# Kernel optimization log

Hardware: AMD Instinct MI355X
Metric: run time of the kernel (lower is better)

The kernel has to match this reference:

```python
import jax, jax.numpy as jnp
import numpy as np

N = 50000          # points
K = 16             # neighbors per query (n_max)
M = N * K          # ragged pair count
DIM = 96
HEADS = 6
HEAD_DIM = DIM // HEADS
WINDOW = 4.0
QUANT = 0.25
QGL = int(WINDOW / QUANT)   # quant_grid_length = 16
SCALE = HEAD_DIM ** -0.5


def setup_inputs() -> dict:
    key = jax.random.key(0)
    ks = jax.random.split(key, 10)
    feats = jax.random.normal(ks[0], (N, DIM), dtype=jnp.float32)
    xyz = jax.random.uniform(ks[1], (N, 3), dtype=jnp.float32) * 8.0
    index_0 = jnp.repeat(jnp.arange(N, dtype=jnp.int32), K)            # sorted query ids
    index_1 = jax.random.randint(ks[2], (M,), 0, N, dtype=jnp.int32)   # neighbor ids
    index_0_offsets = jnp.arange(N + 1, dtype=jnp.int32) * K
    W_qkv = jax.random.normal(ks[3], (DIM, 3 * DIM), dtype=jnp.float32) * 0.02
    b_qkv = jnp.zeros((3 * DIM,), dtype=jnp.float32)
    table_q = jax.random.normal(ks[4], (4 * QGL, HEADS, HEAD_DIM, 3), dtype=jnp.float32) * 0.02
    table_k = jax.random.normal(ks[5], (4 * QGL, HEADS, HEAD_DIM, 3), dtype=jnp.float32) * 0.02
    table_v = jax.random.normal(ks[6], (4 * QGL, HEADS, HEAD_DIM, 3), dtype=jnp.float32) * 0.02
    W_proj = jax.random.normal(ks[7], (DIM, DIM), dtype=jnp.float32) * 0.02
    b_proj = jnp.zeros((DIM,), dtype=jnp.float32)
    return {
        "feats": feats, "xyz": xyz,
        "index_0": index_0, "index_0_offsets": index_0_offsets, "n_max": K,
        "index_1": index_1, "shift_size": jnp.float32(0.0),
        "W_qkv": W_qkv, "b_qkv": b_qkv,
        "table_q": table_q, "table_k": table_k, "table_v": table_v,
        "W_proj": W_proj, "b_proj": b_proj,
    }


def reference(feats, xyz, index_0, index_0_offsets, n_max, index_1, shift_size,
              W_qkv, b_qkv, table_q, table_k, table_v, W_proj, b_proj):
    n = feats.shape[0]
    # qkv projection -> (N, 3, H, HD)
    qkv = (feats @ W_qkv + b_qkv).reshape(n, 3, HEADS, HEAD_DIM)
    q = qkv[:, 0] * SCALE
    k = qkv[:, 1]
    v = qkv[:, 2]

    # step1: per-pair QK dot product (pointops.attention_step1_v2)
    qg = q[index_0]                      # (M, H, HD) gathered by query id
    kg = k[index_1]                      # (M, H, HD) gathered by neighbor id
    attn = jnp.einsum('mhd,mhd->mh', qg, kg)   # (M, H)

    # quantized relative positions
    xyz_quant = jnp.floor(((xyz - xyz.min(axis=0) + shift_size) % WINDOW) / QUANT)
    rel = xyz_quant[index_0] - xyz_quant[index_1]       # (M, 3)
    rel_idx = (rel + (QGL - 1)).astype(jnp.int32)       # map_func, in [0, 2*QGL-2]

    # relative position bias (pointops.dot_prod_with_idx_v3: query + key tables)
    bias = jnp.zeros_like(attn)
    for c in range(3):   # fixed 3 coordinate axes
        tq = table_q[rel_idx[:, c], :, :, c]            # (M, H, HD)
        tk = table_k[rel_idx[:, c], :, :, c]
        bias = bias + jnp.einsum('mhd,mhd->mh', qg, tq) + jnp.einsum('mhd,mhd->mh', kg, tk)
    attn = attn + bias

    # scatter softmax over index_0 segments
    seg_max = jax.ops.segment_max(attn, index_0, num_segments=n)
    e = jnp.exp(attn - seg_max[index_0])
    denom = jax.ops.segment_sum(e, index_0, num_segments=n)
    sm = e / denom[index_0]                              # (M, H)

    # step2 with relative position value (pointops.attention_step2_with_rel_pos_value_v2)
    vg = v[index_1]                                      # (M, H, HD)
    for c in range(3):
        vg = vg + table_v[rel_idx[:, c], :, :, c]
    x = jax.ops.segment_sum(sm[:, :, None] * vg, index_0, num_segments=n)  # (N, H, HD)
    x = x.reshape(n, DIM)
    return x @ W_proj + b_proj
```

## Files before the change

### kernel.cpp

```cpp
#include <hip/hip_runtime.h>
#include <hip/hip_fp16.h>
#include <math.h>

#define FLT_BIG 3.402823466e38f
typedef unsigned int uint;
typedef unsigned short ushort;
typedef __attribute__((ext_vector_type(8))) _Float16 half8;
typedef __attribute__((ext_vector_type(4))) float floatx4;

__device__ inline ushort f2h(float f) {
    return __half_as_ushort(__float2half(f));
}
__device__ inline float dot2(uint a, uint b, float c) {
    float d;
    asm("v_dot2_f32_f16 %0, %1, %2, %3" : "=v"(d) : "v"(a), "v"(b), "v"(c));
    return d;
}
template <int CTRL>
__device__ inline float dppf(float x) {
    return __int_as_float(__builtin_amdgcn_update_dpp(
        __float_as_int(x), __float_as_int(x), CTRL, 0xF, 0xF, true));
}

__global__ void min_reduce_kernel(const float* __restrict__ xyz, int n, float* mn) {
    float m0 = FLT_BIG, m1 = FLT_BIG, m2 = FLT_BIG;
    for (int i = blockIdx.x * blockDim.x + threadIdx.x; i < n; i += gridDim.x * blockDim.x) {
        m0 = fminf(m0, xyz[3 * i + 0]);
        m1 = fminf(m1, xyz[3 * i + 1]);
        m2 = fminf(m2, xyz[3 * i + 2]);
    }
#pragma unroll
    for (int off = 32; off > 0; off >>= 1) {
        m0 = fminf(m0, __shfl_down(m0, off));
        m1 = fminf(m1, __shfl_down(m1, off));
        m2 = fminf(m2, __shfl_down(m2, off));
    }
    if ((threadIdx.x & 63) == 0) {
        atomicMin((int*)&mn[0], __float_as_int(m0));
        atomicMin((int*)&mn[1], __float_as_int(m1));
        atomicMin((int*)&mn[2], __float_as_int(m2));
    }
}

__global__ void prep_kernel(const float* __restrict__ W_qkv,
                            const float* __restrict__ W_proj,
                            const float* __restrict__ tq, const float* __restrict__ tk,
                            const float* __restrict__ tv,
                            ushort* __restrict__ wtqkv, ushort* __restrict__ wtproj,
                            ushort* __restrict__ rq, ushort* __restrict__ rk,
                            ushort* __restrict__ rv, float* mn) {
    int tid = blockIdx.x * 256 + threadIdx.x;
    if (tid < 3) mn[tid] = FLT_BIG;
    if (tid < 18432) {
        int c = tid / 6144, rem = tid - c * 6144;
        int idx = rem / 96, hd = rem - idx * 96;
        int src = (idx * 96 + hd) * 3 + c;
        rq[tid] = f2h(tq[src]);
        rk[tid] = f2h(tk[src]);
        rv[tid] = f2h(tv[src]);
    }
    if (tid < 27648) {
        int j = tid / 96, d = tid - j * 96;
        wtqkv[tid] = f2h(W_qkv[d * 288 + j]);
    }
    if (tid < 9216) {
        int j = tid / 96, d = tid - j * 96;
        wtproj[tid] = f2h(W_proj[d * 96 + j]);
    }
}

__global__ __launch_bounds__(384) void qkv_mfma_kernel(
    const float* __restrict__ A, const ushort* __restrict__ WT,
    const float* __restrict__ bias, uint4* __restrict__ qout4,
    uint4* __restrict__ kvout4, const float* __restrict__ xyz,
    const float* __restrict__ mn, const float* __restrict__ shiftp,
    uint* __restrict__ xq, int n) {
    __shared__ ushort Ash[64 * 104];
    __shared__ ushort lds[6][32 * 112];
    const int t = threadIdx.x;
    const int row0 = blockIdx.x * 64;

    if (t < 64) {
        int rp = row0 + t;
        if (rp < n) {
            float shift = shiftp[0];
            float q0 = floorf(fmodf(xyz[3 * rp + 0] - mn[0] + shift, 4.0f) * 4.0f);
            float q1 = floorf(fmodf(xyz[3 * rp + 1] - mn[1] + shift, 4.0f) * 4.0f);
            float q2 = floorf(fmodf(xyz[3 * rp + 2] - mn[2] + shift, 4.0f) * 4.0f);
            xq[rp] = (uint)(int)q0 | ((uint)(int)q1 << 8) | ((uint)(int)q2 << 16);
        }
    }

    const float4* A4 = (const float4*)A;
#pragma unroll
    for (int j = 0; j < 4; j++) {
        int idx = t + j * 384;
        int row = idx / 24, c4 = idx - row * 24;
        int gr = row0 + row; if (gr > n - 1) gr = n - 1;
        float4 v = A4[(size_t)gr * 24 + c4];
        uint2 pk;
        pk.x = (uint)f2h(v.x) | ((uint)f2h(v.y) << 16);
        pk.y = (uint)f2h(v.z) | ((uint)f2h(v.w) << 16);
        *(uint2*)&Ash[row * 104 + c4 * 4] = pk;
    }
    __syncthreads();

    const int wave = t >> 6, lane = t & 63;
    const int ch = wave >> 1, rg = wave & 1;
    const int m = lane & 15, q = lane >> 4;
    const int wrow0 = row0 + rg * 32;

    const ushort* wbase = WT + ((size_t)ch * 96 + m) * 96 + q * 8;

    floatx4 acc[2][6];
#pragma unroll
    for (int g = 0; g < 2; g++)
#pragma unroll
        for (int ct = 0; ct < 6; ct++) acc[g][ct] = (floatx4){0.f, 0.f, 0.f, 0.f};

#pragma unroll
    for (int kk4 = 0; kk4 < 24; kk4 += 8) {
        half8 a0 = *(const half8*)&Ash[(rg * 32 + m) * 104 + (kk4 + q * 2) * 4];
        half8 a1 = *(const half8*)&Ash[(rg * 32 + 16 + m) * 104 + (kk4 + q * 2) * 4];
#pragma unroll
        for (int ct = 0; ct < 6; ct++) {
            half8 b = *(const half8*)(wbase + ct * 16 * 96 + kk4 * 4);
            acc[0][ct] = __builtin_amdgcn_mfma_f32_16x16x32_f16(a0, b, acc[0][ct], 0, 0, 0);
            acc[1][ct] = __builtin_amdgcn_mfma_f32_16x16x32_f16(a1, b, acc[1][ct], 0, 0, 0);
        }
    }

    ushort* L = lds[wave];
    const float sc = (ch == 0) ? 0.25f : 1.0f;
#pragma unroll
    for (int g = 0; g < 2; g++)
#pragma unroll
        for (int ct = 0; ct < 6; ct++) {
            float bv = bias[ch * 96 + ct * 16 + m];
#pragma unroll
            for (int r = 0; r < 4; r++) {
                int rowl = g * 16 + q * 4 + r;
                L[rowl * 112 + ct * 16 + m] = f2h((acc[g][ct][r] + bv) * sc);
            }
        }
    const int strideU4 = (ch == 0) ? 12 : 24;
    const int offU4 = (ch == 2) ? 12 : 0;
    uint4* dst = (ch == 0) ? qout4 : kvout4;
#pragma unroll
    for (int i = 0; i < 6; i++) {
        int idx = i * 64 + lane;
        int rowl = idx / 12, u4 = idx - rowl * 12;
        int grow = wrow0 + rowl;
        if (grow < n) {
            uint4 val = *(const uint4*)(L + rowl * 112 + u4 * 8);
            dst[(size_t)grow * strideU4 + offU4 + u4] = val;
        }
    }
}

__global__ __launch_bounds__(256) void proj_mfma_kernel(
    const ushort* __restrict__ A, const ushort* __restrict__ WT,
    const float* __restrict__ bias, float* __restrict__ out, int n) {
    const int wave = threadIdx.x >> 6, lane = threadIdx.x & 63;
    const int m = lane & 15, q = lane >> 4;
    const int row0 = blockIdx.x * 128 + wave * 32;
    if (row0 >= n) return;

    const ushort* wbase = WT + (size_t)m * 96 + q * 8;
    int r0 = row0 + m;      if (r0 > n - 1) r0 = n - 1;
    int r1 = row0 + 16 + m; if (r1 > n - 1) r1 = n - 1;

    floatx4 acc[2][6];
#pragma unroll
    for (int g = 0; g < 2; g++)
#pragma unroll
        for (int ct = 0; ct < 6; ct++) acc[g][ct] = (floatx4){0.f, 0.f, 0.f, 0.f};

#pragma unroll
    for (int kk = 0; kk < 96; kk += 32) {
        half8 a0 = *(const half8*)(A + (size_t)r0 * 96 + q * 8 + kk);
        half8 a1 = *(const half8*)(A + (size_t)r1 * 96 + q * 8 + kk);
#pragma unroll
        for (int ct = 0; ct < 6; ct++) {
            half8 b = *(const half8*)(wbase + ct * 16 * 96 + kk);
            acc[0][ct] = __builtin_amdgcn_mfma_f32_16x16x32_f16(a0, b, acc[0][ct], 0, 0, 0);
            acc[1][ct] = __builtin_amdgcn_mfma_f32_16x16x32_f16(a1, b, acc[1][ct], 0, 0, 0);
        }
    }

#pragma unroll
    for (int g = 0; g < 2; g++)
#pragma unroll
        for (int ct = 0; ct < 6; ct++) {
            int col = ct * 16 + m;
            float bv = bias[col];
#pragma unroll
            for (int r = 0; r < 4; r++) {
                int row = row0 + g * 16 + q * 4 + r;
                if (row < n) out[(size_t)row * 96 + col] = acc[g][ct][r] + bv;
            }
        }
}

#define ATTN_NB 256
#define ATTN_B 8
#define TPITCH 208
#define TSIZE  39936
__global__ __launch_bounds__(768) void attn_kernel(
    const ushort* __restrict__ qh, const ushort* __restrict__ kv,
    const uint* __restrict__ xq, const int* __restrict__ index_1,
    const ushort* __restrict__ rq, const ushort* __restrict__ rk,
    const ushort* __restrict__ rv, ushort* __restrict__ xout, int n) {
    __shared__ uint4 ldsraw[7488];
    char* Lb = (char*)ldsraw;

    const int t = threadIdx.x;
    const int pt = t / 96, tp = t - pt * 96;
    const int h = tp >> 4, e = tp & 15;

    const int stride = gridDim.x * ATTN_B;
    const int iters = (n + stride - 1) / stride;

    int pA, jdA; uint xqpA;
    auto PREF_A = [&](int it) {
        pA = (it * gridDim.x + blockIdx.x) * ATTN_B + pt;
        int pc = pA < n ? pA : n - 1;
        jdA = index_1[(size_t)pc * 16 + e];
        xqpA = xq[pc];
    };
    int p, jd; uint xqp, xqj;
    uint4 ka, kb, va, vb, qa, qb;
    auto PREF_B = [&]() {
        p = pA; jd = jdA; xqp = xqpA;
        int pc = p < n ? p : n - 1;
        const ushort* row = kv + (size_t)jd * 192;
        ka = *(const uint4*)(row + h * 16);
        kb = *(const uint4*)(row + h * 16 + 8);
        va = *(const uint4*)(row + 96 + h * 16);
        vb = *(const uint4*)(row + 96 + h * 16 + 8);
        const ushort* qrow = qh + (size_t)pc * 96 + h * 16;
        qa = *(const uint4*)qrow;
        qb = *(const uint4*)(qrow + 8);
        xqj = xq[jd];
    };
    PREF_A(0); PREF_B(); PREF_A(1);

#pragma unroll
    for (int j = 0; j < 9; j++) {
        const uint4* src = (j < 3) ? (const uint4*)rq
                         : (j < 6) ? (const uint4*)rk : (const uint4*)rv;
        int rem = t + (j % 3) * 768;
        int ROW = rem / 12, slot = rem - ROW * 12;
        uint4 val = src[rem];
        *(uint4*)(Lb + (j / 3) * TSIZE + ROW * TPITCH + slot * 16) = val;
    }
    __syncthreads();

    auto LD2 = [&](const char* base, int R, uint4& A, uint4& B) {
        const char* rb = base + R * TPITCH + h * 32;
        A = *(const uint4*)rb;
        B = *(const uint4*)(rb + 16);
    };
    auto F2 = [](const uint4& u, int i) -> float2 {
        return __half22float2(((const __half2*)&u)[i]);
    };

    const bool b3 = (e & 8) != 0, b2 = (e & 4) != 0;
    const bool b1 = (e & 2) != 0, b0 = (e & 1) != 0;

    for (int it = 0; it < iters; it++) {
        const int i0 = (int)(xqp & 255u) - (int)(xqj & 255u) + 15;
        const int i1 = (int)((xqp >> 8) & 255u) - (int)((xqj >> 8) & 255u) + 15;
        const int i2 = (int)((xqp >> 16) & 255u) - (int)((xqj >> 16) & 255u) + 15;

        float f[16];
#pragma unroll
        for (int i = 0; i < 4; i++) {
            float2 lo = F2(va, i), hi = F2(vb, i);
            f[2 * i] = lo.x; f[2 * i + 1] = lo.y;
            f[8 + 2 * i] = hi.x; f[8 + 2 * i + 1] = hi.y;
        }

        float a;
        {
            float x0 = dot2(qa.x, ka.x, 0.f), x1 = dot2(qa.y, ka.y, 0.f);
            x0 = dot2(qa.z, ka.z, x0); x1 = dot2(qa.w, ka.w, x1);
            x0 = dot2(qb.x, kb.x, x0); x1 = dot2(qb.y, kb.y, x1);
            x0 = dot2(qb.z, kb.z, x0); x1 = dot2(qb.w, kb.w, x1);
            float bias = 0.f;
#define BIAS_C(ROW)                                                            \
            {                                                                  \
                uint4 ta, tb, ua, ub;                                          \
                LD2(Lb, (ROW), ta, tb);                                        \
                LD2(Lb + TSIZE, (ROW), ua, ub);                                \
                float u = dot2(qa.x, ta.x, 0.f), w = dot2(ka.x, ua.x, 0.f);    \
                u = dot2(qa.y, ta.y, u); w = dot2(ka.y, ua.y, w);              \
                u = dot2(qa.z, ta.z, u); w = dot2(ka.z, ua.z, w);              \
                u = dot2(qa.w, ta.w, u); w = dot2(ka.w, ua.w, w);              \
                u = dot2(qb.x, tb.x, u); w = dot2(kb.x, ub.x, w);              \
                u = dot2(qb.y, tb.y, u); w = dot2(kb.y, ub.y, w);              \
                u = dot2(qb.z, tb.z, u); w = dot2(kb.z, ub.z, w);              \
                u = dot2(qb.w, tb.w, u); w = dot2(kb.w, ub.w, w);              \
                bias += u + w;                                                 \
            }
            BIAS_C(i0)
            BIAS_C(64 + i1)
            BIAS_C(128 + i2)
#undef BIAS_C
            a = x0 + x1 + bias;
        }

        const int op = p;
        if (it + 1 < iters) { PREF_B(); PREF_A(it + 2); }

        {
            uint4 t0a, t0b, t1a, t1b, t2a, t2b;
            LD2(Lb + 2 * TSIZE, i0, t0a, t0b);
            LD2(Lb + 2 * TSIZE, 64 + i1, t1a, t1b);
            LD2(Lb + 2 * TSIZE, 128 + i2, t2a, t2b);
#pragma unroll
            for (int i = 0; i < 4; i++) {
                float2 a0 = F2(t0a, i), a1 = F2(t1a, i), a2 = F2(t2a, i);
                f[2 * i]     += a0.x + a1.x + a2.x;
                f[2 * i + 1] += a0.y + a1.y + a2.y;
                float2 c0 = F2(t0b, i), c1 = F2(t1b, i), c2 = F2(t2b, i);
                f[8 + 2 * i]     += c0.x + c1.x + c2.x;
                f[8 + 2 * i + 1] += c0.y + c1.y + c2.y;
            }
        }

        float wgt;
        {
            float mx = a;
            mx = fmaxf(mx, dppf<0x128>(mx));
            mx = fmaxf(mx, dppf<0x124>(mx));
            mx = fmaxf(mx, dppf<0x122>(mx));
            mx = fmaxf(mx, dppf<0x121>(mx));
            float ex = __expf(a - mx);
            float sum = ex;
            sum += dppf<0x128>(sum);
            sum += dppf<0x124>(sum);
            sum += dppf<0x122>(sum);
            sum += dppf<0x121>(sum);
            wgt = ex * __builtin_amdgcn_rcpf(sum);
        }

        float P[16];
#pragma unroll
        for (int c = 0; c < 16; c++) P[c] = wgt * f[c];
        float A8[8];
#pragma unroll
        for (int j = 0; j < 8; j++) {
            float kp = b3 ? P[j + 8] : P[j];
            float sd = b3 ? P[j] : P[j + 8];
            A8[j] = kp + dppf<0x140>(sd);
        }
        float B4[4];
#pragma unroll
        for (int j = 0; j < 4; j++) {
            float kp = b2 ? A8[j + 4] : A8[j];
            float sd = b2 ? A8[j] : A8[j + 4];
            B4[j] = kp + dppf<0x141>(sd);
        }
        float C2[2];
#pragma unroll
        for (int j = 0; j < 2; j++) {
            float kp = b1 ? B4[j + 2] : B4[j];
            float sd = b1 ? B4[j] : B4[j + 2];
            C2[j] = kp + dppf<0x4E>(sd);
        }
        {
            float kp = b0 ? C2[1] : C2[0];
            float sd = b0 ? C2[0] : C2[1];
            float xres = kp + dppf<0xB1>(sd);
            if (op < n) xout[(size_t)op * 96 + tp] = f2h(xres);
        }
    }
}

extern "C" void kernel_launch(void* const* d_in, const int* in_sizes, int n_in,
                              void* d_out, int out_size, void* d_ws, size_t ws_size,
                              hipStream_t stream) {
    const float* feats   = (const float*)d_in[0];
    const float* xyz     = (const float*)d_in[1];
    const int*   index_1 = (const int*)d_in[5];
    const float* shiftp  = (const float*)d_in[6];
    const float* W_qkv   = (const float*)d_in[7];
    const float* b_qkv   = (const float*)d_in[8];
    const float* table_q = (const float*)d_in[9];
    const float* table_k = (const float*)d_in[10];
    const float* table_v = (const float*)d_in[11];
    const float* W_proj  = (const float*)d_in[12];
    const float* b_proj  = (const float*)d_in[13];
    float* out = (float*)d_out;

    const int n = in_sizes[0] / 96;

    float* w = (float*)d_ws;
    float*  mn     = w;
    ushort* qbf    = (ushort*)(w + 16);
    ushort* kvbuf  = qbf + (size_t)n * 96;
    ushort* xbuf   = kvbuf + (size_t)n * 192;
    ushort* wtqkv  = xbuf + (size_t)n * 96;
    ushort* wtproj = wtqkv + 27648;
    ushort* rq     = wtproj + 9216;
    ushort* rk     = rq + 18432;
    ushort* rv     = rk + 18432;
    uint*   xqv    = (uint*)(rv + 18432);

    prep_kernel<<<108, 256, 0, stream>>>(W_qkv, W_proj, table_q, table_k, table_v,
                                         wtqkv, wtproj, rq, rk, rv, mn);
    min_reduce_kernel<<<256, 256, 0, stream>>>(xyz, n, mn);
    qkv_mfma_kernel<<<(n + 63) / 64, 384, 0, stream>>>(feats, wtqkv, b_qkv,
                                                       (uint4*)qbf, (uint4*)kvbuf,
                                                       xyz, mn, shiftp, xqv, n);
    attn_kernel<<<ATTN_NB, 768, 0, stream>>>(qbf, kvbuf, xqv, index_1, rq, rk,
                                             rv, xbuf, n);
    proj_mfma_kernel<<<(n + 127) / 128, 256, 0, stream>>>(xbuf, wtproj, b_proj,
                                                          out, n);
}
```

Before: 225.6 us.

## Fuse output projection into attention kernel and merge min-reduce into prep

The attention kernel now keeps each block's per-point outputs in shared memory instead of writing them to global memory. At the end it runs the MFMA output projection on them, writing final rows through the strided point-to-block mapping. This removes the separate projection launch and the fp16 intermediate round trip. The xyz min-reduction is folded into the weight/table prep kernel, with a memset to initialise the minima, which removes another launch. The V table pitch changes, and shared-memory use grows to about 158KB. The projection tail also runs serially after all attention iterations in each block.

```diff
diff --git a/kernel.cpp b/kernel.cpp
--- a/kernel.cpp
+++ b/kernel.cpp
@@ -22,35 +22,15 @@
         __float_as_int(x), __float_as_int(x), CTRL, 0xF, 0xF, true));
 }
 
-__global__ void min_reduce_kernel(const float* __restrict__ xyz, int n, float* mn) {
-    float m0 = FLT_BIG, m1 = FLT_BIG, m2 = FLT_BIG;
-    for (int i = blockIdx.x * blockDim.x + threadIdx.x; i < n; i += gridDim.x * blockDim.x) {
-        m0 = fminf(m0, xyz[3 * i + 0]);
-        m1 = fminf(m1, xyz[3 * i + 1]);
-        m2 = fminf(m2, xyz[3 * i + 2]);
-    }
-#pragma unroll
-    for (int off = 32; off > 0; off >>= 1) {
-        m0 = fminf(m0, __shfl_down(m0, off));
-        m1 = fminf(m1, __shfl_down(m1, off));
-        m2 = fminf(m2, __shfl_down(m2, off));
-    }
-    if ((threadIdx.x & 63) == 0) {
-        atomicMin((int*)&mn[0], __float_as_int(m0));
-        atomicMin((int*)&mn[1], __float_as_int(m1));
-        atomicMin((int*)&mn[2], __float_as_int(m2));
-    }
-}
-
-__global__ void prep_kernel(const float* __restrict__ W_qkv,
-                            const float* __restrict__ W_proj,
-                            const float* __restrict__ tq, const float* __restrict__ tk,
-                            const float* __restrict__ tv,
-                            ushort* __restrict__ wtqkv, ushort* __restrict__ wtproj,
-                            ushort* __restrict__ rq, ushort* __restrict__ rk,
-                            ushort* __restrict__ rv, float* mn) {
+__global__ void prep_min_kernel(const float* __restrict__ W_qkv,
+                                const float* __restrict__ W_proj,
+                                const float* __restrict__ tq, const float* __restrict__ tk,
+                                const float* __restrict__ tv,
+                                const float* __restrict__ xyz,
+                                ushort* __restrict__ wtqkv, ushort* __restrict__ wtproj,
+                                ushort* __restrict__ rq, ushort* __restrict__ rk,
+                                ushort* __restrict__ rv, float* mn, int n) {
     int tid = blockIdx.x * 256 + threadIdx.x;
-    if (tid < 3) mn[tid] = FLT_BIG;
     if (tid < 18432) {
         int c = tid / 6144, rem = tid - c * 6144;
         int idx = rem / 96, hd = rem - idx * 96;
@@ -66,6 +46,23 @@
     if (tid < 9216) {
         int j = tid / 96, d = tid - j * 96;
         wtproj[tid] = f2h(W_proj[d * 96 + j]);
+    }
+    float m0 = FLT_BIG, m1 = FLT_BIG, m2 = FLT_BIG;
+    for (int i = tid; i < n; i += gridDim.x * 256) {
+        m0 = fminf(m0, xyz[3 * i + 0]);
+        m1 = fminf(m1, xyz[3 * i + 1]);
+        m2 = fminf(m2, xyz[3 * i + 2]);
+    }
+#pragma unroll
+    for (int off = 32; off > 0; off >>= 1) {
+        m0 = fminf(m0, __shfl_down(m0, off));
+        m1 = fminf(m1, __shfl_down(m1, off));
+        m2 = fminf(m2, __shfl_down(m2, off));
+    }
+    if ((threadIdx.x & 63) == 0) {
+        atomicMin((int*)&mn[0], __float_as_int(m0));
+        atomicMin((int*)&mn[1], __float_as_int(m1));
+        atomicMin((int*)&mn[2], __float_as_int(m2));
     }
 }
 
@@ -158,72 +155,32 @@
     }
 }
 
-__global__ __launch_bounds__(256) void proj_mfma_kernel(
-    const ushort* __restrict__ A, const ushort* __restrict__ WT,
-    const float* __restrict__ bias, float* __restrict__ out, int n) {
-    const int wave = threadIdx.x >> 6, lane = threadIdx.x & 63;
-    const int m = lane & 15, q = lane >> 4;
-    const int row0 = blockIdx.x * 128 + wave * 32;
-    if (row0 >= n) return;
-
-    const ushort* wbase = WT + (size_t)m * 96 + q * 8;
-    int r0 = row0 + m;      if (r0 > n - 1) r0 = n - 1;
-    int r1 = row0 + 16 + m; if (r1 > n - 1) r1 = n - 1;
-
-    floatx4 acc[2][6];
-#pragma unroll
-    for (int g = 0; g < 2; g++)
-#pragma unroll
-        for (int ct = 0; ct < 6; ct++) acc[g][ct] = (floatx4){0.f, 0.f, 0.f, 0.f};
-
-#pragma unroll
-    for (int kk = 0; kk < 96; kk += 32) {
-        half8 a0 = *(const half8*)(A + (size_t)r0 * 96 + q * 8 + kk);
-        half8 a1 = *(const half8*)(A + (size_t)r1 * 96 + q * 8 + kk);
-#pragma unroll
-        for (int ct = 0; ct < 6; ct++) {
-            half8 b = *(const half8*)(wbase + ct * 16 * 96 + kk);
-            acc[0][ct] = __builtin_amdgcn_mfma_f32_16x16x32_f16(a0, b, acc[0][ct], 0, 0, 0);
-            acc[1][ct] = __builtin_amdgcn_mfma_f32_16x16x32_f16(a1, b, acc[1][ct], 0, 0, 0);
-        }
-    }
-
-#pragma unroll
-    for (int g = 0; g < 2; g++)
-#pragma unroll
-        for (int ct = 0; ct < 6; ct++) {
-            int col = ct * 16 + m;
-            float bv = bias[col];
-#pragma unroll
-            for (int r = 0; r < 4; r++) {
-                int row = row0 + g * 16 + q * 4 + r;
-                if (row < n) out[(size_t)row * 96 + col] = acc[g][ct][r] + bv;
-            }
-        }
-}
-
 #define ATTN_NB 256
 #define ATTN_B 8
-#define TPITCH 208
-#define TSIZE  39936
-__global__ __launch_bounds__(768) void attn_kernel(
+#define QPITCH 208
+#define VPITCH 192
+#define KOFF 39936
+#define VOFF 79872
+#define XOFF 116736
+#define XPITCH 104
+__global__ __launch_bounds__(768) void attn_proj_kernel(
     const ushort* __restrict__ qh, const ushort* __restrict__ kv,
     const uint* __restrict__ xq, const int* __restrict__ index_1,
     const ushort* __restrict__ rq, const ushort* __restrict__ rk,
-    const ushort* __restrict__ rv, ushort* __restrict__ xout, int n) {
-    __shared__ uint4 ldsraw[7488];
-    char* Lb = (char*)ldsraw;
-
-    const int t = threadIdx.x;
+    const ushort* __restrict__ rv, const ushort* __restrict__ wtproj,
+    const float* __restrict__ b_proj, float* __restrict__ out, int n) {
+    __shared__ __align__(16) char Lb[158336];
+
+    const int t = threadIdx.x, b = blockIdx.x;
     const int pt = t / 96, tp = t - pt * 96;
     const int h = tp >> 4, e = tp & 15;
 
-    const int stride = gridDim.x * ATTN_B;
+    const int stride = ATTN_NB * ATTN_B;
     const int iters = (n + stride - 1) / stride;
 
     int pA, jdA; uint xqpA;
     auto PREF_A = [&](int it) {
-        pA = (it * gridDim.x + blockIdx.x) * ATTN_B + pt;
+        pA = (it * ATTN_NB + b) * ATTN_B + pt;
         int pc = pA < n ? pA : n - 1;
         jdA = index_1[(size_t)pc * 16 + e];
         xqpA = xq[pc];
@@ -247,17 +204,20 @@
 
 #pragma unroll
     for (int j = 0; j < 9; j++) {
-        const uint4* src = (j < 3) ? (const uint4*)rq
-                         : (j < 6) ? (const uint4*)rk : (const uint4*)rv;
+        const int tbl = j / 3;
+        const uint4* src = (tbl == 0) ? (const uint4*)rq
+                         : (tbl == 1) ? (const uint4*)rk : (const uint4*)rv;
         int rem = t + (j % 3) * 768;
         int ROW = rem / 12, slot = rem - ROW * 12;
         uint4 val = src[rem];
-        *(uint4*)(Lb + (j / 3) * TSIZE + ROW * TPITCH + slot * 16) = val;
+        const int base = (tbl == 0) ? 0 : (tbl == 1) ? KOFF : VOFF;
+        const int pitch = (tbl == 2) ? VPITCH : QPITCH;
+        *(uint4*)(Lb + base + ROW * pitch + slot * 16) = val;
     }
     __syncthreads();
 
-    auto LD2 = [&](const char* base, int R, uint4& A, uint4& B) {
-        const char* rb = base + R * TPITCH + h * 32;
+    auto LD2Q = [&](const char* base, int R, uint4& A, uint4& B) {
+        const char* rb = base + R * QPITCH + h * 32;
         A = *(const uint4*)rb;
         B = *(const uint4*)(rb + 16);
     };
@@ -291,8 +251,8 @@
 #define BIAS_C(ROW)                                                            \
             {                                                                  \
                 uint4 ta, tb, ua, ub;                                          \
-                LD2(Lb, (ROW), ta, tb);                                        \
-                LD2(Lb + TSIZE, (ROW), ua, ub);                                \
+                LD2Q(Lb, (ROW), ta, tb);                                       \
+                LD2Q(Lb + KOFF, (ROW), ua, ub);                                \
                 float u = dot2(qa.x, ta.x, 0.f), w = dot2(ka.x, ua.x, 0.f);    \
                 u = dot2(qa.y, ta.y, u); w = dot2(ka.y, ua.y, w);              \
                 u = dot2(qa.z, ta.z, u); w = dot2(ka.z, ua.z, w);              \
@@ -310,14 +270,22 @@
             a = x0 + x1 + bias;
         }
 
-        const int op = p;
         if (it + 1 < iters) { PREF_B(); PREF_A(it + 2); }
 
         {
             uint4 t0a, t0b, t1a, t1b, t2a, t2b;
-            LD2(Lb + 2 * TSIZE, i0, t0a, t0b);
-            LD2(Lb + 2 * TSIZE, 64 + i1, t1a, t1b);
-            LD2(Lb + 2 * TSIZE, 128 + i2, t2a, t2b);
+            {
+                const char* rb = Lb + VOFF + i0 * VPITCH + h * 32;
+                t0a = *(const uint4*)rb; t0b = *(const uint4*)(rb + 16);
+            }
+            {
+                const char* rb = Lb + VOFF + (64 + i1) * VPITCH + h * 32;
+                t1a = *(const uint4*)rb; t1b = *(const uint4*)(rb + 16);
+            }
+            {
+                const char* rb = Lb + VOFF + (128 + i2) * VPITCH + h * 32;
+                t2a = *(const uint4*)rb; t2b = *(const uint4*)(rb + 16);
+            }
 #pragma unroll
             for (int i = 0; i < 4; i++) {
                 float2 a0 = F2(t0a, i), a1 = F2(t1a, i), a2 = F2(t2a, i);
@@ -373,7 +341,54 @@
             float kp = b0 ? C2[1] : C2[0];
             float sd = b0 ? C2[0] : C2[1];
             float xres = kp + dppf<0xB1>(sd);
-            if (op < n) xout[(size_t)op * 96 + tp] = f2h(xres);
+            *(ushort*)(Lb + XOFF + (it * ATTN_B + pt) * (XPITCH * 2) + tp * 2) =
+                f2h(xres);
+        }
+    }
+    __syncthreads();
+
+    {
+        const int wave = t >> 6, lane = t & 63;
+        const int m = lane & 15, q = lane >> 4;
+        const int row0l = wave * 32;
+        const int nloc = iters * ATTN_B;
+        if (row0l < nloc) {
+            const ushort* X = (const ushort*)(Lb + XOFF);
+            const ushort* wbase = wtproj + (size_t)m * 96 + q * 8;
+            int r0 = row0l + m;      if (r0 > nloc - 1) r0 = nloc - 1;
+            int r1 = row0l + 16 + m; if (r1 > nloc - 1) r1 = nloc - 1;
+            floatx4 acc[2][6];
+#pragma unroll
+            for (int g = 0; g < 2; g++)
+#pragma unroll
+                for (int ct = 0; ct < 6; ct++) acc[g][ct] = (floatx4){0.f, 0.f, 0.f, 0.f};
+#pragma unroll
+            for (int kk = 0; kk < 96; kk += 32) {
+                half8 a0 = *(const half8*)(X + r0 * XPITCH + q * 8 + kk);
+                half8 a1 = *(const half8*)(X + r1 * XPITCH + q * 8 + kk);
+#pragma unroll
+                for (int ct = 0; ct < 6; ct++) {
+                    half8 bb = *(const half8*)(wbase + ct * 16 * 96 + kk);
+                    acc[0][ct] = __builtin_amdgcn_mfma_f32_16x16x32_f16(a0, bb, acc[0][ct], 0, 0, 0);
+                    acc[1][ct] = __builtin_amdgcn_mfma_f32_16x16x32_f16(a1, bb, acc[1][ct], 0, 0, 0);
+                }
+            }
+#pragma unroll
+            for (int g = 0; g < 2; g++)
+#pragma unroll
+                for (int ct = 0; ct < 6; ct++) {
+                    int col = ct * 16 + m;
+                    float bv = b_proj[col];
+#pragma unroll
+                    for (int r = 0; r < 4; r++) {
+                        int lr = row0l + g * 16 + q * 4 + r;
+                        if (lr < nloc) {
+                            int grow = (lr >> 3) * stride + b * ATTN_B + (lr & 7);
+                            if (grow < n)
+                                out[(size_t)grow * 96 + col] = acc[g][ct][r] + bv;
+                        }
+                    }
+                }
         }
     }
 }
@@ -400,22 +415,21 @@
     float*  mn     = w;
     ushort* qbf    = (ushort*)(w + 16);
     ushort* kvbuf  = qbf + (size_t)n * 96;
-    ushort* xbuf   = kvbuf + (size_t)n * 192;
-    ushort* wtqkv  = xbuf + (size_t)n * 96;
+    ushort* wtqkv  = kvbuf + (size_t)n * 192;
     ushort* wtproj = wtqkv + 27648;
     ushort* rq     = wtproj + 9216;
     ushort* rk     = rq + 18432;
     ushort* rv     = rk + 18432;
     uint*   xqv    = (uint*)(rv + 18432);
 
-    prep_kernel<<<108, 256, 0, stream>>>(W_qkv, W_proj, table_q, table_k, table_v,
-                                         wtqkv, wtproj, rq, rk, rv, mn);
-    min_reduce_kernel<<<256, 256, 0, stream>>>(xyz, n, mn);
+    hipMemsetAsync(mn, 0x7F, 3 * sizeof(float), stream);
+    prep_min_kernel<<<108, 256, 0, stream>>>(W_qkv, W_proj, table_q, table_k,
+                                             table_v, xyz, wtqkv, wtproj,
+                                             rq, rk, rv, mn, n);
     qkv_mfma_kernel<<<(n + 63) / 64, 384, 0, stream>>>(feats, wtqkv, b_qkv,
                                                        (uint4*)qbf, (uint4*)kvbuf,
                                                        xyz, mn, shiftp, xqv, n);
-    attn_kernel<<<ATTN_NB, 768, 0, stream>>>(qbf, kvbuf, xqv, index_1, rq, rk,
-                                             rv, xbuf, n);
-    proj_mfma_kernel<<<(n + 127) / 128, 256, 0, stream>>>(xbuf, wtproj, b_proj,
-                                                          out, n);
-}
+    attn_proj_kernel<<<ATTN_NB, 768, 0, stream>>>(qbf, kvbuf, xqv, index_1,
+                                                  rq, rk, rv, wtproj, b_proj,
+                                                  out, n);
+}
```

Result: faster. 200.7 us (-11.1%).
